# Optimization experiments

Hardware: AMD Instinct MI355X
Metric: run time of the kernel (lower is better)

Reference implementation:

```python
import jax, jax.numpy as jnp
import numpy as np

KS, PAD = 3, 1  # AttentionConv kernel_size=3, padding=1, stride=1, groups=1


def _unfold(t, H, W):
    # t: [B, C, H+2*PAD, W+2*PAD] -> [B, C, H, W, KS*KS] local windows
    return jnp.stack([t[:, :, i:i + H, j:j + W]
                      for i in range(KS) for j in range(KS)], axis=-1)


def _attn_conv(x, wq, bq, wk, bk, wv, bv, rh, rw):
    # SASA local self-attention conv. x: [B, Cin, H, W]; wq/wk/wv: [Cout, Cin]
    B, Cin, H, W = x.shape
    q = jnp.einsum('bchw,oc->bohw', x, wq) + bq[None, :, None, None]
    xp = jnp.pad(x, ((0, 0), (0, 0), (PAD, PAD), (PAD, PAD)))
    k = jnp.einsum('bchw,oc->bohw', xp, wk) + bk[None, :, None, None]
    v = jnp.einsum('bchw,oc->bohw', xp, wv) + bv[None, :, None, None]
    k = _unfold(k, H, W)  # [B, Cout, H, W, 9]
    v = _unfold(v, H, W)
    Ch = rh.shape[0]  # Cout // 2
    # relative embeddings: first channel half gets rel_h (varies along kh),
    # second half gets rel_w (varies along kw)
    rel = jnp.concatenate([
        jnp.broadcast_to(rh[:, :, None], (Ch, KS, KS)),
        jnp.broadcast_to(rw[:, None, :], (Ch, KS, KS)),
    ], axis=0).reshape(2 * Ch, KS * KS)
    k = k + rel[None, :, None, None, :]
    attn = jax.nn.softmax(q[..., None] * k, axis=-1)  # per-channel softmax over window
    return jnp.einsum('bchwk,bchwk->bchw', attn, v)


def setup_inputs() -> dict:
    key = jax.random.key(0)
    ks = jax.random.split(key, 16)
    B, Cin, Cout = 4, 256, 512
    S, F, O = 64500, 489, 140
    inp = {
        'p3': jax.random.normal(ks[0], (B, Cin, 64, 64), jnp.float32),
        'p4': jax.random.normal(ks[1], (B, Cin, 32, 32), jnp.float32),
        'p5': jax.random.normal(ks[2], (B, Cin, 16, 16), jnp.float32),
        'wq': jax.random.normal(ks[3], (3, Cout, Cin), jnp.float32) * 0.01,
        'bq': jnp.zeros((3, Cout), jnp.float32),
        'wk': jax.random.normal(ks[4], (3, Cout, Cin), jnp.float32) * 0.01,
        'bk': jnp.zeros((3, Cout), jnp.float32),
        'wv': jax.random.normal(ks[5], (3, Cout, Cin), jnp.float32) * 0.01,
        'bv': jnp.zeros((3, Cout), jnp.float32),
        'rel_h': jax.random.normal(ks[6], (3, Cout // 2, KS), jnp.float32),
        'rel_w': jax.random.normal(ks[7], (3, Cout // 2, KS), jnp.float32),
        'ws': jax.random.normal(ks[8], (S, Cout), jnp.float32) * 0.01,
        'bs': jnp.zeros((S,), jnp.float32),
        'wf': jax.random.normal(ks[9], (F, Cout), jnp.float32) * 0.01,
        'bf': jnp.zeros((F,), jnp.float32),
        'wo': jax.random.normal(ks[10], (O, Cout), jnp.float32) * 0.01,
        'bo': jnp.zeros((O,), jnp.float32),
    }
    return inp


def reference(p3, p4, p5, wq, bq, wk, bk, wv, bv, rel_h, rel_w,
              ws, bs, wf, bf, wo, bo):
    feat = 0.
    for i, x in enumerate((p3, p4, p5)):
        y = _attn_conv(x, wq[i], bq[i], wk[i], bk[i], wv[i], bv[i],
                       rel_h[i], rel_w[i])
        y = jax.nn.relu(y)
        feat = feat + y.mean(axis=(2, 3))  # AdaptiveAvgPool2d((1,1)) -> [B, 512]
    # 1x1 conv classifiers on [B, 512, 1, 1] == dense layers; .view(N, -1)
    logits_species = feat @ ws.T + bs
    logits_family = feat @ wf.T + bf
    logits_order = feat @ wo.T + bo
    return (logits_species, logits_family, logits_order)
```

## Files before the change

### kernel.cpp

```cpp
#include <hip/hip_runtime.h>
#include <hip/hip_bf16.h>
#include <stdint.h>

typedef __bf16 bf16x8 __attribute__((ext_vector_type(8)));
typedef float  f32x4  __attribute__((ext_vector_type(4)));
typedef unsigned short u16x8 __attribute__((ext_vector_type(8)));
typedef unsigned int   u32x4 __attribute__((ext_vector_type(4)));

#define LOG2E 1.4426950408889634f

__device__ __forceinline__ unsigned short f2bf(float f) {
    union { float f; unsigned u; } v; v.f = f;
    unsigned r = v.u + 0x7fffu + ((v.u >> 16) & 1u);
    return (unsigned short)(r >> 16);
}
__device__ __forceinline__ float lo16(unsigned d) {
    union { unsigned u; float f; } v; v.u = d << 16; return v.f;
}
__device__ __forceinline__ float hi16(unsigned d) {
    union { unsigned u; float f; } v; v.u = d & 0xffff0000u; return v.f;
}
__device__ __forceinline__ float fexp2(float x) {
    float r; asm("v_exp_f32 %0, %1" : "=v"(r) : "v"(x)); return r;
}
__device__ __forceinline__ float frcp(float x) {
    float r; asm("v_rcp_f32 %0, %1" : "=v"(r) : "v"(x)); return r;
}

__device__ __forceinline__ void async16(void* lds, const void* g) {
    __builtin_amdgcn_global_load_lds(
        (const __attribute__((address_space(1))) unsigned int*)g,
        (__attribute__((address_space(3))) unsigned int*)lds, 16, 0, 0);
}

#define NT_ALL   21504
#define OFF_L1   16384
#define OFF_L2   20480

__global__ __launch_bounds__(256) void prep_kernel(
    const float* __restrict__ x0, const float* __restrict__ x1,
    const float* __restrict__ x2,
    const float* __restrict__ wq, const float* __restrict__ wk,
    const float* __restrict__ wv,
    unsigned short* __restrict__ wb, unsigned short* __restrict__ xT,
    float* __restrict__ feat)
{
    __shared__ unsigned short tile[64][65];
    int bid = blockIdx.x;
    if (bid == 0) {
        for (int i = threadIdx.x; i < 2048; i += 256) feat[i] = 0.f;
        return;
    }
    bid -= 1;
    if (bid < 576) {
        int t = bid / 192;
        int i = ((bid % 192) * 256 + threadIdx.x) * 8;
        const float* src = (t == 0) ? wq : (t == 1) ? wk : wv;
        f32x4 a = *(const f32x4*)(src + i);
        f32x4 b = *(const f32x4*)(src + i + 4);
        u16x8 o;
        o[0] = f2bf(a.x); o[1] = f2bf(a.y); o[2] = f2bf(a.z); o[3] = f2bf(a.w);
        o[4] = f2bf(b.x); o[5] = f2bf(b.y); o[6] = f2bf(b.z); o[7] = f2bf(b.w);
        *(u16x8*)(wb + (size_t)t * 393216 + i) = o;
        return;
    }
    bid -= 576;
    int xb = bid % 84;
    int c0 = ((bid / 84) & 3) * 64;
    int b  = bid / 336;
    const float* xp; int tb, HW, lvl_off;
    if (xb < 64)      { xp = x0; tb = xb;      HW = 4096; lvl_off = 0;      }
    else if (xb < 80) { xp = x1; tb = xb - 64; HW = 1024; lvl_off = OFF_L1; }
    else              { xp = x2; tb = xb - 80; HW = 256;  lvl_off = OFF_L2; }
    int hw0 = tb * 64;
    xp += (size_t)b * 256 * HW;
    int tx = threadIdx.x & 63;
    int ty = threadIdx.x >> 6;
#pragma unroll
    for (int i = 0; i < 16; ++i) {
        int c = c0 + ty * 16 + i;
        tile[ty * 16 + i][tx] = f2bf(xp[(size_t)c * HW + hw0 + tx]);
    }
    __syncthreads();
    unsigned short* op = xT + ((size_t)lvl_off + (size_t)b * HW + hw0) * 256 + c0;
#pragma unroll
    for (int i = 0; i < 16; ++i) {
        int r = ty * 16 + i;
        op[(size_t)r * 256 + tx] = tile[tx][r];
    }
}

__global__ __launch_bounds__(256, 4) void qkv_gemm_kernel(
    const unsigned short* __restrict__ wb,
    const float* __restrict__ bq, const float* __restrict__ bk,
    const float* __restrict__ bv,
    const unsigned short* __restrict__ xT,
    unsigned short* __restrict__ qkv)
{
    int bid = blockIdx.x;
    int swz = (bid & 7) * 252 + (bid >> 3);
    int nt  = swz / 12;
    int mz  = swz % 12;
    int z   = mz >> 2;
    int bm0 = (mz & 3) * 128;
    int bn0 = nt * 128;
    int lvl = (bn0 >= OFF_L2) ? 2 : (bn0 >= OFF_L1) ? 1 : 0;
    const unsigned short* Wm = wb + ((size_t)z * 3 + lvl) * 131072;
    const float* bias = ((z == 0) ? bq : (z == 1) ? bk : bv) + lvl * 512;
    unsigned short* out = qkv + (size_t)z * 512 * NT_ALL;

    __shared__ unsigned short smem[2][8192];

    int tid  = threadIdx.x;
    int lane = tid & 63;
    int wid  = tid >> 6;
    int wr   = wid >> 1, wc = wid & 1;
    int l15  = lane & 15;
    int kg   = lane >> 4;

    f32x4 acc[4][4];
#pragma unroll
    for (int i = 0; i < 4; ++i)
#pragma unroll
        for (int j = 0; j < 4; ++j) acc[i][j] = (f32x4){0.f, 0.f, 0.f, 0.f};

    int aRow0 = bm0 + (2 * wid)     * 16 + l15;
    int aRow1 = bm0 + (2 * wid + 1) * 16 + l15;
    int bRow0 = bn0 + (2 * wid)     * 16 + l15;
    int bRow1 = bn0 + (2 * wid + 1) * 16 + l15;
    int kbase = kg * 8;

    auto STAGE = [&](int t, int bufi) {
        int kk = t * 32 + kbase;
        unsigned short* As = smem[bufi];
        unsigned short* Bs = As + 4096;
        async16(As + (2 * wid)     * 512, Wm + (size_t)aRow0 * 256 + kk);
        async16(As + (2 * wid + 1) * 512, Wm + (size_t)aRow1 * 256 + kk);
        async16(Bs + (2 * wid)     * 512, xT + (size_t)bRow0 * 256 + kk);
        async16(Bs + (2 * wid + 1) * 512, xT + (size_t)bRow1 * 256 + kk);
    };

    STAGE(0, 0);
    __syncthreads();

    for (int it = 0; it < 8; ++it) {
        if (it < 7) STAGE(it + 1, (it + 1) & 1);
        const unsigned short* As = smem[it & 1];
        const unsigned short* Bs = As + 4096;
        bf16x8 af[4], bg[4];
#pragma unroll
        for (int mi = 0; mi < 4; ++mi)
            af[mi] = *reinterpret_cast<const bf16x8*>(As + ((wr * 4 + mi) * 64 + lane) * 8);
#pragma unroll
        for (int ni = 0; ni < 4; ++ni)
            bg[ni] = *reinterpret_cast<const bf16x8*>(Bs + ((wc * 4 + ni) * 64 + lane) * 8);
#pragma unroll
        for (int mi = 0; mi < 4; ++mi)
#pragma unroll
            for (int ni = 0; ni < 4; ++ni)
                acc[mi][ni] = __builtin_amdgcn_mfma_f32_16x16x32_bf16(
                    af[mi], bg[ni], acc[mi][ni], 0, 0, 0);
        __syncthreads();
    }

    unsigned short* T = smem[0];
#pragma unroll
    for (int p = 0; p < 2; ++p) {
        __syncthreads();
#pragma unroll
        for (int s = 0; s < 2; ++s) {
            int mi = 2 * p + s;
            int qw = wr * 32 + s * 16 + kg * 4;
            int ow = bm0 + wr * 64 + mi * 16 + kg * 4;
#pragma unroll
            for (int ni = 0; ni < 4; ++ni) {
                int cn = wc * 64 + ni * 16 + l15;
#pragma unroll
                for (int r = 0; r < 4; ++r)
                    T[(qw + r) * 136 + cn] = f2bf(acc[mi][ni][r] + bias[ow + r]);
            }
        }
        __syncthreads();
        int q  = tid >> 2;
        int j4 = tid & 3;
        int o  = bm0 + (q >> 5) * 64 + (2 * p + ((q >> 4) & 1)) * 16 + (q & 15);
        unsigned short* orow = out + (size_t)o * NT_ALL + bn0;
#pragma unroll
        for (int c = 0; c < 4; ++c) {
            int nl = c * 32 + j4 * 8;
            *(u16x8*)(orow + nl) = *(const u16x8*)(T + q * 136 + nl);
        }
    }
}

__global__ __launch_bounds__(256, 4) void attn_kernel(
    const unsigned short* __restrict__ qkv,
    const float* __restrict__ bk, const float* __restrict__ bv,
    const float* __restrict__ relh, const float* __restrict__ relw,
    float* __restrict__ feat)
{
    int id = blockIdx.x;
    int c  = (id & 7) * 64 + (id >> 3) / 11;
    int xb = (id >> 3) % 11;
    int lvl, lgW, lvl_off, hw_all;
    if (xb < 8)       { lvl = 0; lgW = 6; lvl_off = 0;      hw_all = xb * 2048 + threadIdx.x * 8; }
    else if (xb < 10) { lvl = 1; lgW = 5; lvl_off = OFF_L1; hw_all = (xb - 8) * 2048 + threadIdx.x * 8; }
    else              { lvl = 2; lgW = 4; lvl_off = OFF_L2; hw_all = threadIdx.x * 8; }
    int W = 1 << lgW, H = W, HW = W << lgW;
    bool active = hw_all < 4 * HW;
    int b  = hw_all >> (2 * lgW);
    int hw = hw_all & (HW - 1);
    int h = hw >> lgW, w0 = hw & (W - 1);

    size_t n0 = (size_t)lvl_off + hw_all;
    const unsigned short* qp = qkv + (size_t)c          * NT_ALL + n0;
    const unsigned short* kp = qkv + ((size_t)512 + c)  * NT_ALL + n0;
    const unsigned short* vp = qkv + ((size_t)1024 + c) * NT_ALL + n0;

    float bkc = bk[lvl * 512 + c], bvc = bv[lvl * 512 + c];
    bool ish = (c < 256);
    const float* rsp = ish ? (relh + lvl * 768 + c * 3)
                           : (relw + lvl * 768 + (c - 256) * 3);
    float rs0 = rsp[0], rs1 = rsp[1], rs2 = rsp[2];

    float ysum = 0.f;
    if (active) {
        float kf[3][10], vf[3][10];
        u32x4 qv = *(const u32x4*)qp;
        float qf[8];
#pragma unroll
        for (int d = 0; d < 4; ++d) { qf[2 * d] = lo16(qv[d]); qf[2 * d + 1] = hi16(qv[d]); }
#pragma unroll
        for (int r = 0; r < 3; ++r) {
            int y = h + r - 1;
            if ((unsigned)y < (unsigned)H) {
                int off = (r - 1) << lgW;
                u32x4 kv = *(const u32x4*)(kp + off);
                u32x4 vv = *(const u32x4*)(vp + off);
#pragma unroll
                for (int d = 0; d < 4; ++d) {
                    kf[r][1 + 2 * d] = lo16(kv[d]); kf[r][2 + 2 * d] = hi16(kv[d]);
                    vf[r][1 + 2 * d] = lo16(vv[d]); vf[r][2 + 2 * d] = hi16(vv[d]);
                }
                bool hasL = (w0 > 0), hasR = (w0 + 8 < W);
                kf[r][0] = hasL ? hi16(*(const unsigned*)(kp + off - 2)) : bkc;
                vf[r][0] = hasL ? hi16(*(const unsigned*)(vp + off - 2)) : bvc;
                kf[r][9] = hasR ? lo16(*(const unsigned*)(kp + off + 8)) : bkc;
                vf[r][9] = hasR ? lo16(*(const unsigned*)(vp + off + 8)) : bvc;
            } else {
#pragma unroll
                for (int j = 0; j < 10; ++j) { kf[r][j] = bkc; vf[r][j] = bvc; }
            }
        }
#define ROW(r, q0, q1, q2)                                         \
        {                                                          \
            float p0 = fexp2(fmaf(qln, kf[r][j + 0], q0));         \
            float p1 = fexp2(fmaf(qln, kf[r][j + 1], q1));         \
            float p2 = fexp2(fmaf(qln, kf[r][j + 2], q2));         \
            num = fmaf(p0, vf[r][j + 0], num);                     \
            num = fmaf(p1, vf[r][j + 1], num);                     \
            num = fmaf(p2, vf[r][j + 2], num);                     \
            den += p0 + p1 + p2;                                   \
        }
        if (ish) {
#pragma unroll
            for (int j = 0; j < 8; ++j) {
                float qln = qf[j] * LOG2E;
                float pr0 = qln * rs0, pr1 = qln * rs1, pr2 = qln * rs2;
                float num = 0.f, den = 0.f;
                ROW(0, pr0, pr0, pr0)
                ROW(1, pr1, pr1, pr1)
                ROW(2, pr2, pr2, pr2)
                ysum += fmaxf(num * frcp(den), 0.f);
            }
        } else {
#pragma unroll
            for (int j = 0; j < 8; ++j) {
                float qln = qf[j] * LOG2E;
                float pr0 = qln * rs0, pr1 = qln * rs1, pr2 = qln * rs2;
                float num = 0.f, den = 0.f;
                ROW(0, pr0, pr1, pr2)
                ROW(1, pr0, pr1, pr2)
                ROW(2, pr0, pr1, pr2)
                ysum += fmaxf(num * frcp(den), 0.f);
            }
        }
#undef ROW
        ysum *= (1.0f / HW);
    }
#pragma unroll
    for (int off = 16; off; off >>= 1) ysum += __shfl_down(ysum, off, 32);
    if (active && ((threadIdx.x & 31) == 0))
        atomicAdd(&feat[(size_t)b * 512 + c], ysum);
}

__global__ __launch_bounds__(256, 4) void logits_kernel(
    const float* __restrict__ feat,
    const float* __restrict__ ws, const float* __restrict__ bs,
    const float* __restrict__ wf, const float* __restrict__ bff,
    const float* __restrict__ wo, const float* __restrict__ bo,
    float* __restrict__ out)
{
    int lane = threadIdx.x & 63;
    int wid  = threadIdx.x >> 6;
    f32x4 fr[4][2];
#pragma unroll
    for (int b = 0; b < 4; ++b) {
        fr[b][0] = *(const f32x4*)(feat + b * 512 + lane * 4);
        fr[b][1] = *(const f32x4*)(feat + b * 512 + 256 + lane * 4);
    }
    const int ROWS = 64500 + 489 + 140;
    for (int row = blockIdx.x * 4 + wid; row < ROWS; row += 8192) {
        const float* wm; float bias; size_t obase; int ostride;
        if (row < 64500) {
            wm = ws + (size_t)row * 512; bias = bs[row]; obase = (size_t)row; ostride = 64500;
        } else if (row < 64500 + 489) {
            int r = row - 64500;
            wm = wf + (size_t)r * 512; bias = bff[r]; obase = 258000 + (size_t)r; ostride = 489;
        } else {
            int r = row - 64989;
            wm = wo + (size_t)r * 512; bias = bo[r]; obase = 259956 + (size_t)r; ostride = 140;
        }
        f32x4 w1 = *(const f32x4*)(wm + lane * 4);
        f32x4 w2 = *(const f32x4*)(wm + 256 + lane * 4);
        float accs[4];
#pragma unroll
        for (int b = 0; b < 4; ++b) {
            f32x4 f1 = fr[b][0], f2 = fr[b][1];
            accs[b] = w1.x * f1.x + w1.y * f1.y + w1.z * f1.z + w1.w * f1.w
                    + w2.x * f2.x + w2.y * f2.y + w2.z * f2.z + w2.w * f2.w;
        }
#pragma unroll
        for (int off = 32; off; off >>= 1)
#pragma unroll
            for (int b = 0; b < 4; ++b) accs[b] += __shfl_down(accs[b], off, 64);
        if (lane == 0)
#pragma unroll
            for (int b = 0; b < 4; ++b) out[obase + (size_t)b * ostride] = accs[b] + bias;
    }
}

extern "C" void kernel_launch(void* const* d_in, const int* in_sizes, int n_in,
                              void* d_out, int out_size, void* d_ws, size_t ws_size,
                              hipStream_t stream)
{
    const float* x0  = (const float*)d_in[0];
    const float* x1  = (const float*)d_in[1];
    const float* x2  = (const float*)d_in[2];
    const float* wq  = (const float*)d_in[3];
    const float* bq  = (const float*)d_in[4];
    const float* wk  = (const float*)d_in[5];
    const float* bk  = (const float*)d_in[6];
    const float* wv  = (const float*)d_in[7];
    const float* bv  = (const float*)d_in[8];
    const float* relh = (const float*)d_in[9];
    const float* relw = (const float*)d_in[10];
    const float* ws  = (const float*)d_in[11];
    const float* bs  = (const float*)d_in[12];
    const float* wf  = (const float*)d_in[13];
    const float* bff = (const float*)d_in[14];
    const float* wo  = (const float*)d_in[15];
    const float* bo  = (const float*)d_in[16];
    float* out = (float*)d_out;

    char* wsb = (char*)d_ws;
    float* feat = (float*)wsb;
    unsigned short* wb = (unsigned short*)(wsb + 8192);
    unsigned short* xT = (unsigned short*)(wsb + 8192 + 2359296);
    unsigned short* qkv = (unsigned short*)(wsb + 8192 + 2359296 + 11010048);

    prep_kernel<<<dim3(1 + 576 + 1344), 256, 0, stream>>>(
        x0, x1, x2, wq, wk, wv, wb, xT, feat);
    qkv_gemm_kernel<<<dim3(2016), 256, 0, stream>>>(
        wb, bq, bk, bv, xT, qkv);
    attn_kernel<<<dim3(5632), 256, 0, stream>>>(
        qkv, bk, bv, relh, relw, feat);
    logits_kernel<<<dim3(2048), 256, 0, stream>>>(feat, ws, bs, wf, bff, wo, bo, out);
}
```

Before: 111.9 us.

## Compute two output rows per thread in attention kernel to reuse K/V rows

Each thread in the local attention kernel now handles a 2-row by 8-column patch and loads 4 K/V rows instead of 3 rows per output row, so neighbouring rows share loaded halo data. The block-to-work mapping is rebuilt: one block per (channel, batch) at level 0, and one block per channel covering all batches at levels 1 and 2. The grid drops from 5632 to 3072 blocks, and the level-2 block uses only 64 active threads. The reduction uses 64-wide or 16-wide shuffles with fewer atomics. This trades more registers per thread and idle lanes in the level-2 blocks for less global load traffic and fewer atomics.

```diff
diff --git a/kernel.cpp b/kernel.cpp
--- a/kernel.cpp
+++ b/kernel.cpp
@@ -199,20 +199,27 @@
     const float* __restrict__ relh, const float* __restrict__ relw,
     float* __restrict__ feat)
 {
-    int id = blockIdx.x;
-    int c  = (id & 7) * 64 + (id >> 3) / 11;
-    int xb = (id >> 3) % 11;
-    int lvl, lgW, lvl_off, hw_all;
-    if (xb < 8)       { lvl = 0; lgW = 6; lvl_off = 0;      hw_all = xb * 2048 + threadIdx.x * 8; }
-    else if (xb < 10) { lvl = 1; lgW = 5; lvl_off = OFF_L1; hw_all = (xb - 8) * 2048 + threadIdx.x * 8; }
-    else              { lvl = 2; lgW = 4; lvl_off = OFF_L2; hw_all = threadIdx.x * 8; }
+    int id  = blockIdx.x;
+    int c   = (id & 7) * 64 + (id >> 3) / 6;
+    int xb  = (id >> 3) % 6;
+    int tid = threadIdx.x;
+    int lvl, lgW, lvl_off, b, pair, w0, rwidth;
+    bool active = true;
+    if (xb < 4) {
+        lvl = 0; lgW = 6; lvl_off = 0;      b = xb;
+        pair = tid >> 3; w0 = (tid & 7) * 8; rwidth = 64;
+    } else if (xb == 4) {
+        lvl = 1; lgW = 5; lvl_off = OFF_L1; b = tid >> 6;
+        pair = (tid & 63) >> 2; w0 = (tid & 3) * 8; rwidth = 64;
+    } else {
+        lvl = 2; lgW = 4; lvl_off = OFF_L2; b = (tid >> 4) & 3;
+        pair = (tid & 15) >> 1; w0 = (tid & 1) * 8; rwidth = 16;
+        active = tid < 64;
+    }
     int W = 1 << lgW, H = W, HW = W << lgW;
-    bool active = hw_all < 4 * HW;
-    int b  = hw_all >> (2 * lgW);
-    int hw = hw_all & (HW - 1);
-    int h = hw >> lgW, w0 = hw & (W - 1);
-
-    size_t n0 = (size_t)lvl_off + hw_all;
+    int h0 = 2 * pair;
+
+    size_t n0 = (size_t)lvl_off + (size_t)b * HW + (h0 << lgW) + w0;
     const unsigned short* qp = qkv + (size_t)c          * NT_ALL + n0;
     const unsigned short* kp = qkv + ((size_t)512 + c)  * NT_ALL + n0;
     const unsigned short* vp = qkv + ((size_t)1024 + c) * NT_ALL + n0;
@@ -225,14 +232,11 @@
 
     float ysum = 0.f;
     if (active) {
-        float kf[3][10], vf[3][10];
-        u32x4 qv = *(const u32x4*)qp;
-        float qf[8];
-#pragma unroll
-        for (int d = 0; d < 4; ++d) { qf[2 * d] = lo16(qv[d]); qf[2 * d + 1] = hi16(qv[d]); }
-#pragma unroll
-        for (int r = 0; r < 3; ++r) {
-            int y = h + r - 1;
+        bool hasL = (w0 > 0), hasR = (w0 + 8 < W);
+        float kf[4][10], vf[4][10];
+#pragma unroll
+        for (int r = 0; r < 4; ++r) {
+            int y = h0 + r - 1;
             if ((unsigned)y < (unsigned)H) {
                 int off = (r - 1) << lgW;
                 u32x4 kv = *(const u32x4*)(kp + off);
@@ -242,7 +246,6 @@
                     kf[r][1 + 2 * d] = lo16(kv[d]); kf[r][2 + 2 * d] = hi16(kv[d]);
                     vf[r][1 + 2 * d] = lo16(vv[d]); vf[r][2 + 2 * d] = hi16(vv[d]);
                 }
-                bool hasL = (w0 > 0), hasR = (w0 + 8 < W);
                 kf[r][0] = hasL ? hi16(*(const unsigned*)(kp + off - 2)) : bkc;
                 vf[r][0] = hasL ? hi16(*(const unsigned*)(vp + off - 2)) : bvc;
                 kf[r][9] = hasR ? lo16(*(const unsigned*)(kp + off + 8)) : bkc;
@@ -252,46 +255,62 @@
                 for (int j = 0; j < 10; ++j) { kf[r][j] = bkc; vf[r][j] = bvc; }
             }
         }
-#define ROW(r, q0, q1, q2)                                         \
+#define ROW(rw, q0, q1, q2)                                        \
         {                                                          \
-            float p0 = fexp2(fmaf(qln, kf[r][j + 0], q0));         \
-            float p1 = fexp2(fmaf(qln, kf[r][j + 1], q1));         \
-            float p2 = fexp2(fmaf(qln, kf[r][j + 2], q2));         \
-            num = fmaf(p0, vf[r][j + 0], num);                     \
-            num = fmaf(p1, vf[r][j + 1], num);                     \
-            num = fmaf(p2, vf[r][j + 2], num);                     \
+            float p0 = fexp2(fmaf(qln, kf[rw][j + 0], q0));        \
+            float p1 = fexp2(fmaf(qln, kf[rw][j + 1], q1));        \
+            float p2 = fexp2(fmaf(qln, kf[rw][j + 2], q2));        \
+            num = fmaf(p0, vf[rw][j + 0], num);                    \
+            num = fmaf(p1, vf[rw][j + 1], num);                    \
+            num = fmaf(p2, vf[rw][j + 2], num);                    \
             den += p0 + p1 + p2;                                   \
         }
-        if (ish) {
-#pragma unroll
-            for (int j = 0; j < 8; ++j) {
-                float qln = qf[j] * LOG2E;
-                float pr0 = qln * rs0, pr1 = qln * rs1, pr2 = qln * rs2;
-                float num = 0.f, den = 0.f;
-                ROW(0, pr0, pr0, pr0)
-                ROW(1, pr1, pr1, pr1)
-                ROW(2, pr2, pr2, pr2)
-                ysum += fmaxf(num * frcp(den), 0.f);
+#pragma unroll
+        for (int orow = 0; orow < 2; ++orow) {
+            u32x4 qv = *(const u32x4*)(qp + (orow << lgW));
+            float qf[8];
+#pragma unroll
+            for (int d = 0; d < 4; ++d) {
+                qf[2 * d] = lo16(qv[d]); qf[2 * d + 1] = hi16(qv[d]);
             }
-        } else {
-#pragma unroll
-            for (int j = 0; j < 8; ++j) {
-                float qln = qf[j] * LOG2E;
-                float pr0 = qln * rs0, pr1 = qln * rs1, pr2 = qln * rs2;
-                float num = 0.f, den = 0.f;
-                ROW(0, pr0, pr1, pr2)
-                ROW(1, pr0, pr1, pr2)
-                ROW(2, pr0, pr1, pr2)
-                ysum += fmaxf(num * frcp(den), 0.f);
+            if (ish) {
+#pragma unroll
+                for (int j = 0; j < 8; ++j) {
+                    float qln = qf[j] * LOG2E;
+                    float pr0 = qln * rs0, pr1 = qln * rs1, pr2 = qln * rs2;
+                    float num = 0.f, den = 0.f;
+                    ROW(orow + 0, pr0, pr0, pr0)
+                    ROW(orow + 1, pr1, pr1, pr1)
+                    ROW(orow + 2, pr2, pr2, pr2)
+                    ysum += fmaxf(num * frcp(den), 0.f);
+                }
+            } else {
+#pragma unroll
+                for (int j = 0; j < 8; ++j) {
+                    float qln = qf[j] * LOG2E;
+                    float pr0 = qln * rs0, pr1 = qln * rs1, pr2 = qln * rs2;
+                    float num = 0.f, den = 0.f;
+                    ROW(orow + 0, pr0, pr1, pr2)
+                    ROW(orow + 1, pr0, pr1, pr2)
+                    ROW(orow + 2, pr0, pr1, pr2)
+                    ysum += fmaxf(num * frcp(den), 0.f);
+                }
             }
         }
 #undef ROW
         ysum *= (1.0f / HW);
     }
-#pragma unroll
-    for (int off = 16; off; off >>= 1) ysum += __shfl_down(ysum, off, 32);
-    if (active && ((threadIdx.x & 31) == 0))
-        atomicAdd(&feat[(size_t)b * 512 + c], ysum);
+    if (rwidth == 64) {
+#pragma unroll
+        for (int off = 32; off; off >>= 1) ysum += __shfl_down(ysum, off, 64);
+        if (active && ((tid & 63) == 0))
+            atomicAdd(&feat[(size_t)b * 512 + c], ysum);
+    } else {
+#pragma unroll
+        for (int off = 8; off; off >>= 1) ysum += __shfl_down(ysum, off, 16);
+        if (active && ((tid & 15) == 0))
+            atomicAdd(&feat[(size_t)b * 512 + c], ysum);
+    }
 }
 
 __global__ __launch_bounds__(256, 4) void logits_kernel(
@@ -373,7 +392,7 @@
         x0, x1, x2, wq, wk, wv, wb, xT, feat);
     qkv_gemm_kernel<<<dim3(2016), 256, 0, stream>>>(
         wb, bq, bk, bv, xT, qkv);
-    attn_kernel<<<dim3(5632), 256, 0, stream>>>(
+    attn_kernel<<<dim3(3072), 256, 0, stream>>>(
         qkv, bk, bv, relh, relw, feat);
     logits_kernel<<<dim3(2048), 256, 0, stream>>>(feat, ws, bs, wf, bff, wo, bo, out);
 }
```

After: 108.3 us. 1.03x faster.
